# Kernel optimization log

Measured on AMD Instinct MI355X. Metric: run time of the kernel, lower is better.

Reference implementation:

```python
import jax, jax.numpy as jnp
import numpy as np

EMBED_DIM = 1024
NUM_HEADS = 16
HEAD_DIM = EMBED_DIM // NUM_HEADS
B, QL, CL = 2, 2048, 2048


def setup_inputs() -> dict:
    key = jax.random.key(0)
    ks = jax.random.split(key, 10)
    s = 1.0 / np.sqrt(EMBED_DIM)  # torch Linear default init scale (approx)
    inp = {
        "query": jax.random.normal(ks[0], (B, QL, EMBED_DIM), jnp.float32),
        "context": jax.random.normal(ks[1], (B, CL, EMBED_DIM), jnp.float32),
        "Wq": jax.random.normal(ks[2], (EMBED_DIM, EMBED_DIM), jnp.float32) * s,
        "bq": jnp.zeros((EMBED_DIM,), jnp.float32),
        "Wk": jax.random.normal(ks[3], (EMBED_DIM, EMBED_DIM), jnp.float32) * s,
        "bk": jnp.zeros((EMBED_DIM,), jnp.float32),
        "Wv": jax.random.normal(ks[4], (EMBED_DIM, EMBED_DIM), jnp.float32) * s,
        "bv": jnp.zeros((EMBED_DIM,), jnp.float32),
        "Wo": jax.random.normal(ks[5], (EMBED_DIM, EMBED_DIM), jnp.float32) * s,
        "bo": jnp.zeros((EMBED_DIM,), jnp.float32),
    }
    return inp


def reference(query, context, Wq, bq, Wk, bk, Wv, bv, Wo, bo):
    b, ql, _ = query.shape
    cl = context.shape[1]
    # projections (torch Linear: x @ W.T + b; here W stored as (in, out) so x @ W + b)
    Q = (query @ Wq + bq).reshape(b, ql, NUM_HEADS, HEAD_DIM).transpose(0, 2, 1, 3)
    K = (context @ Wk + bk).reshape(b, cl, NUM_HEADS, HEAD_DIM).transpose(0, 2, 1, 3)
    V = (context @ Wv + bv).reshape(b, cl, NUM_HEADS, HEAD_DIM).transpose(0, 2, 1, 3)
    # scores [b, h, ql, cl]
    scores = jnp.einsum("bhqd,bhkd->bhqk", Q, K) / np.sqrt(HEAD_DIM).astype(np.float32)
    probs = jax.nn.softmax(scores, axis=-1)
    # dropout=0.0 (eval): identity
    attended = jnp.einsum("bhqk,bhkd->bhqd", probs, V)
    attended = attended.transpose(0, 2, 1, 3).reshape(b, ql, EMBED_DIM)
    return attended @ Wo + bo
```

## Files before the change

### kernel.cpp

```cpp
#include <hip/hip_runtime.h>
#include <hip/hip_bf16.h>
#include <stdint.h>

#define EMBED 1024
#define NH 16
#define HD 64
#define BATCH 2
#define QLEN 2048
#define CLEN 2048

typedef short short8 __attribute__((ext_vector_type(8)));
typedef unsigned short ushort8v __attribute__((ext_vector_type(8)));
typedef float f32x4 __attribute__((ext_vector_type(4)));
typedef float f32x16 __attribute__((ext_vector_type(16)));
typedef uint32_t u32x4 __attribute__((ext_vector_type(4)));

#define QSCALE 0.18033688f

__device__ __forceinline__ void async_load16(const void* g, void* l) {
    __builtin_amdgcn_global_load_lds((const __attribute__((address_space(1))) void*)g,
                                     (__attribute__((address_space(3))) void*)l, 16, 0, 0);
}

__device__ __forceinline__ uint32_t pack2(float a, float b) {
    float2 f{a, b};
    __hip_bfloat162 t = __float22bfloat162_rn(f);
    uint32_t u;
    __builtin_memcpy(&u, &t, 4);
    return u;
}

__global__ void prep(const float* __restrict__ query, const float* __restrict__ context,
                     __hip_bfloat16* __restrict__ qbf, __hip_bfloat16* __restrict__ cbf,
                     const float* __restrict__ W0, const float* __restrict__ W1,
                     const float* __restrict__ W2, const float* __restrict__ W3,
                     __hip_bfloat16* __restrict__ T0, __hip_bfloat16* __restrict__ T1,
                     __hip_bfloat16* __restrict__ T2, __hip_bfloat16* __restrict__ T3) {
    const int y = blockIdx.y;
    const int tid = threadIdx.x;
    if (y < 2) {
        const float* src = y ? context : query;
        __hip_bfloat16* dst = y ? cbf : qbf;
#pragma unroll
        for (int k = 0; k < 4; k++) {
            const int i = (blockIdx.x * 1024 + k * 256 + tid) * 4;
            float4 v = *(const float4*)(src + i);
            __hip_bfloat16 h[4];
            h[0] = __float2bfloat16(v.x);
            h[1] = __float2bfloat16(v.y);
            h[2] = __float2bfloat16(v.z);
            h[3] = __float2bfloat16(v.w);
            *(ushort4*)(dst + i) = *(const ushort4*)h;
        }
    } else {
        const int z = y - 2;
        const float* W = z == 0 ? W0 : z == 1 ? W1 : z == 2 ? W2 : W3;
        __hip_bfloat16* Wt = z == 0 ? T0 : z == 1 ? T1 : z == 2 ? T2 : T3;
        __shared__ float t[32][33];
        const int tx = tid & 31, ty = tid >> 5;
        const int n0 = (blockIdx.x & 31) * 32, k0 = (blockIdx.x >> 5) * 32;
#pragma unroll
        for (int r = 0; r < 4; r++)
            t[ty * 4 + r][tx] = W[(size_t)(k0 + ty * 4 + r) * EMBED + n0 + tx];
        __syncthreads();
#pragma unroll
        for (int r = 0; r < 4; r++)
            Wt[(size_t)(n0 + ty * 4 + r) * EMBED + k0 + tx] = __float2bfloat16(t[tx][ty * 4 + r]);
    }
}

__device__ __forceinline__ void gemm128_acc(
    const __hip_bfloat16* __restrict__ A, const __hip_bfloat16* __restrict__ Bt,
    int m0, int n0, __hip_bfloat16* As, __hip_bfloat16* Bs, f32x4 acc[4][4]) {
    const int K = EMBED;
    const int tid = threadIdx.x;
    const int wave = __builtin_amdgcn_readfirstlane(tid >> 6);
    const int lane = tid & 63, l15 = lane & 15, quad = lane >> 4;
    const int wm = (wave >> 1) * 64, wn = (wave & 1) * 64;
    const int srow = tid >> 2, sseg = (tid & 3) * 8;
    for (int k0 = 0; k0 < K; k0 += 32) {
        __syncthreads();
#pragma unroll
        for (int s = 0; s < 2; s++) {
            async_load16(A + (size_t)(m0 + s * 64 + srow) * K + k0 + sseg,
                         As + (size_t)(s * 256 + wave * 64) * 8);
            async_load16(Bt + (size_t)(n0 + s * 64 + srow) * K + k0 + sseg,
                         Bs + (size_t)(s * 256 + wave * 64) * 8);
        }
        __syncthreads();
        short8 af[4], bf[4];
#pragma unroll
        for (int t = 0; t < 4; t++) {
            af[t] = *(const short8*)(As + (wm + t * 16 + l15) * 32 + quad * 8);
            bf[t] = *(const short8*)(Bs + (wn + t * 16 + l15) * 32 + quad * 8);
        }
#pragma unroll
        for (int mt = 0; mt < 4; mt++)
#pragma unroll
            for (int nt = 0; nt < 4; nt++)
                acc[mt][nt] = __builtin_amdgcn_mfma_f32_16x16x32_bf16(af[mt], bf[nt], acc[mt][nt], 0, 0, 0);
    }
}

__global__ __launch_bounds__(256, 3) void proj128(
    const __hip_bfloat16* __restrict__ qbf, const __hip_bfloat16* __restrict__ cbf,
    const __hip_bfloat16* __restrict__ Wqt, const __hip_bfloat16* __restrict__ Wkvt,
    const float* __restrict__ bq, const float* __restrict__ bk, const float* __restrict__ bv,
    __hip_bfloat16* __restrict__ Qp, __hip_bfloat16* __restrict__ Kp, __hip_bfloat16* __restrict__ Vtr) {
    __shared__ __hip_bfloat16 smem[8704];
    __hip_bfloat16* As = smem;
    __hip_bfloat16* Bs = smem + 4096;
    const int j = blockIdx.x;
    const int blk = (j & 7) * 96 + (j >> 3);
    const __hip_bfloat16 *A, *Bt;
    int m0, n0;
    if (blk < 256) {
        A = qbf; Bt = Wqt; m0 = (blk >> 3) * 128; n0 = (blk & 7) * 128;
    } else {
        const int f = blk - 256;
        A = cbf; Bt = Wkvt; m0 = (f >> 4) * 128; n0 = (f & 15) * 128;
    }
    f32x4 acc[4][4] = {};
    gemm128_acc(A, Bt, m0, n0, As, Bs, acc);

    const int tid = threadIdx.x;
    const int wave = __builtin_amdgcn_readfirstlane(tid >> 6);
    const int lane = tid & 63, l15 = lane & 15, quad = lane >> 4;
    const int wm = (wave >> 1) * 64, wn = (wave & 1) * 64;

    if (blk >= 256 && n0 >= 1024) {
        const int cb = n0 - 1024;
        const int b2 = m0 >> 11;
        const int tokb = m0 & 2047;
        __hip_bfloat16* T = smem;
#pragma unroll
        for (int hh = 0; hh < 2; hh++) {
            __syncthreads();
            if ((wn >> 6) == hh) {
#pragma unroll
                for (int nt = 0; nt < 4; nt++) {
                    const int cn = nt * 16 + l15;
                    const float bvv = bv[cb + hh * 64 + cn];
#pragma unroll
                    for (int mt = 0; mt < 4; mt++) {
                        const int m = wm + mt * 16 + quad * 4;
                        __hip_bfloat16 vb[4];
#pragma unroll
                        for (int r = 0; r < 4; r++) vb[r] = __float2bfloat16(acc[mt][nt][r] + bvv);
                        *(ushort4*)(T + cn * 136 + m) = *(const ushort4*)vb;
                    }
                }
            }
            __syncthreads();
            const int r = tid >> 2;
            const int seg = (tid & 3) * 32;
            unsigned short* dst = (unsigned short*)Vtr +
                (size_t)(b2 * 1024 + cb + hh * 64 + r) * CLEN + tokb + seg;
            const unsigned short* srcp = (const unsigned short*)(T + r * 136 + seg);
#pragma unroll
            for (int u = 0; u < 4; u++)
                *(ushort8v*)(dst + u * 8) = *(const ushort8v*)(srcp + u * 8);
        }
    } else {
        const bool isQ = (blk < 256);
        const float* bias = isQ ? bq : bk;
        __hip_bfloat16* C = isQ ? Qp : Kp;
        const float sc = isQ ? QSCALE : 1.0f;
#pragma unroll
        for (int mt = 0; mt < 4; mt++) {
#pragma unroll
            for (int nt = 0; nt < 4; nt++) {
                const int c = n0 + wn + nt * 16 + l15;
                const float bvv = bias[c];
                const int r0 = m0 + wm + mt * 16 + quad * 4;
#pragma unroll
                for (int r = 0; r < 4; r++)
                    C[(size_t)(r0 + r) * 1024 + c] = __float2bfloat16((acc[mt][nt][r] + bvv) * sc);
            }
        }
    }
}

__global__ __launch_bounds__(256, 4) void oproj(
    const __hip_bfloat16* __restrict__ A, const __hip_bfloat16* __restrict__ Bt,
    const float* __restrict__ bias, float* __restrict__ C) {
    __shared__ __hip_bfloat16 As[64 * 32];
    __shared__ __hip_bfloat16 Bs[128 * 32];
    const int K = EMBED, N = EMBED;
    const int j = blockIdx.x;
    const int L = (j & 7) * 64 + (j >> 3);
    const int m0 = (L >> 3) * 64, n0 = (L & 7) * 128;
    const int tid = threadIdx.x;
    const int wave = __builtin_amdgcn_readfirstlane(tid >> 6);
    const int lane = tid & 63, l15 = lane & 15, quad = lane >> 4;
    const int wm = (wave & 1) * 32, wn = (wave >> 1) * 64;
    const int srow = tid >> 2, sseg = (tid & 3) * 8;
    f32x4 acc[2][4] = {};
    for (int k0 = 0; k0 < K; k0 += 32) {
        __syncthreads();
        async_load16(A + (size_t)(m0 + srow) * K + k0 + sseg, As + (size_t)(wave * 64) * 8);
#pragma unroll
        for (int s = 0; s < 2; s++)
            async_load16(Bt + (size_t)(n0 + s * 64 + srow) * K + k0 + sseg,
                         Bs + (size_t)(s * 256 + wave * 64) * 8);
        __syncthreads();
        short8 af[2], bf[4];
#pragma unroll
        for (int t = 0; t < 2; t++)
            af[t] = *(const short8*)(As + (wm + t * 16 + l15) * 32 + quad * 8);
#pragma unroll
        for (int t = 0; t < 4; t++)
            bf[t] = *(const short8*)(Bs + (wn + t * 16 + l15) * 32 + quad * 8);
#pragma unroll
        for (int mt = 0; mt < 2; mt++)
#pragma unroll
            for (int nt = 0; nt < 4; nt++)
                acc[mt][nt] = __builtin_amdgcn_mfma_f32_16x16x32_bf16(af[mt], bf[nt], acc[mt][nt], 0, 0, 0);
    }
#pragma unroll
    for (int mt = 0; mt < 2; mt++) {
#pragma unroll
        for (int nt = 0; nt < 4; nt++) {
            const int c = n0 + wn + nt * 16 + l15;
            const float bvv = bias[c];
            const int r0 = m0 + wm + mt * 16 + quad * 4;
#pragma unroll
            for (int r = 0; r < 4; r++)
                C[(size_t)(r0 + r) * N + c] = acc[mt][nt][r] + bvv;
        }
    }
}

__global__ __launch_bounds__(256, 4) void flash_attn(
    const __hip_bfloat16* __restrict__ Q, const __hip_bfloat16* __restrict__ K,
    const __hip_bfloat16* __restrict__ Vt, __hip_bfloat16* __restrict__ O) {
    __shared__ __hip_bfloat16 Ks[2][64 * 64];
    __shared__ __hip_bfloat16 Vs[2][64 * 64];
    const int tid = threadIdx.x;
    const int wave = __builtin_amdgcn_readfirstlane(tid >> 6);
    const int wq = wave & 1, wc = wave >> 1;
    const int lane = tid & 63, l31 = lane & 31, hbit = lane >> 5;
    const int j = blockIdx.x;
    const int L = (j & 7) * 128 + (j >> 3);
    const int hy = L >> 5;
    const int b = hy >> 4, h = hy & 15;
    const int q0 = (L & 31) * 64;
    const size_t kbase = (size_t)b * CLEN * EMBED + (size_t)h * HD;
    const size_t vtbase = (size_t)((b * NH + h) * HD) * CLEN;
    const int srow8 = lane >> 3;
    const int sgb = (lane & 7) ^ srow8;
    __hip_bfloat16* stK = Ks[wc];
    __hip_bfloat16* stV = Vs[wc];

    const __hip_bfloat16* qptr =
        Q + (size_t)(b * QLEN + q0 + wq * 32 + l31) * EMBED + h * HD + hbit * 8;
    short8 qf[4];
#pragma unroll
    for (int t = 0; t < 4; t++) qf[t] = *(const short8*)(qptr + t * 16);

    f32x16 o[2] = {};
    float lsum = 0.f;
    const int cbase = wc * (CLEN / 2);

    for (int t = 0; t < 16; ++t) {
        const int c0 = cbase + t * 64;
        __syncthreads();
        if (wq == 0) {
#pragma unroll
            for (int i = 0; i < 8; i++)
                async_load16(K + kbase + (size_t)(c0 + i * 8 + srow8) * EMBED + (sgb ^ i) * 8,
                             stK + i * 512);
        } else {
#pragma unroll
            for (int i = 0; i < 8; i++)
                async_load16(Vt + vtbase + (size_t)(i * 8 + srow8) * CLEN + c0 + (sgb ^ i) * 8,
                             stV + i * 512);
        }
        __syncthreads();

#pragma unroll
        for (int mc = 0; mc < 2; mc++) {
            const int row = mc * 32 + l31;
            const int rsw = (row & 7) ^ (row >> 3);
            const __hip_bfloat16* kr = stK + row * 64;
            f32x16 s = {};
#pragma unroll
            for (int kc = 0; kc < 4; kc++) {
                short8 kf = *(const short8*)(kr + ((2 * kc + hbit) ^ rsw) * 8);
                s = __builtin_amdgcn_mfma_f32_32x32x16_bf16(kf, qf[kc], s, 0, 0, 0);
            }
            uint32_t dw[8];
#pragma unroll
            for (int i = 0; i < 8; i++) {
                const float p0 = __builtin_amdgcn_exp2f(s[2 * i]);
                const float p1 = __builtin_amdgcn_exp2f(s[2 * i + 1]);
                lsum += p0 + p1;
                dw[i] = pack2(p0, p1);
            }
#pragma unroll
            for (int tp = 0; tp < 2; tp++) {
                u32x4 fb;
#if __has_builtin(__builtin_amdgcn_permlane32_swap)
                {
                    auto s02 = __builtin_amdgcn_permlane32_swap(dw[4 * tp + 0], dw[4 * tp + 2], false, false);
                    auto s13 = __builtin_amdgcn_permlane32_swap(dw[4 * tp + 1], dw[4 * tp + 3], false, false);
                    fb[0] = s02[0];
                    fb[1] = s13[0];
                    fb[2] = s02[1];
                    fb[3] = s13[1];
                }
#else
                {
                    const uint32_t a0 = hbit ? dw[4 * tp + 2] : dw[4 * tp + 0];
                    const uint32_t a1 = hbit ? dw[4 * tp + 3] : dw[4 * tp + 1];
                    const uint32_t b0 = hbit ? dw[4 * tp + 0] : dw[4 * tp + 2];
                    const uint32_t b1 = hbit ? dw[4 * tp + 1] : dw[4 * tp + 3];
                    const uint32_t x0 = (uint32_t)__shfl_xor((int)b0, 32);
                    const uint32_t x1 = (uint32_t)__shfl_xor((int)b1, 32);
                    fb[0] = hbit ? x0 : a0;
                    fb[1] = hbit ? x1 : a1;
                    fb[2] = hbit ? a0 : x0;
                    fb[3] = hbit ? a1 : x1;
                }
#endif
                const short8 pfr = __builtin_bit_cast(short8, fb);
                const int kc2 = mc * 2 + tp;
#pragma unroll
                for (int dm = 0; dm < 2; dm++) {
                    const int vrow = dm * 32 + l31;
                    const int vsw = (vrow & 7) ^ (vrow >> 3);
                    short8 vf = *(const short8*)(stV + vrow * 64 + ((2 * kc2 + hbit) ^ vsw) * 8);
                    o[dm] = __builtin_amdgcn_mfma_f32_32x32x16_bf16(vf, pfr, o[dm], 0, 0, 0);
                }
            }
        }
    }

    __syncthreads();
    float4* scr4 = (float4*)&Ks[0][0];
    float* scrl = (float*)&Vs[0][0];
    if (wc == 1) {
#pragma unroll
        for (int i = 0; i < 8; i++) {
            float4 c4;
            c4.x = o[i >> 2][(i & 3) * 4 + 0];
            c4.y = o[i >> 2][(i & 3) * 4 + 1];
            c4.z = o[i >> 2][(i & 3) * 4 + 2];
            c4.w = o[i >> 2][(i & 3) * 4 + 3];
            scr4[i * 128 + wq * 64 + lane] = c4;
        }
        scrl[wq * 64 + lane] = lsum;
    }
    __syncthreads();
    if (wc == 0) {
        lsum += scrl[wq * 64 + lane];
#pragma unroll
        for (int i = 0; i < 8; i++) {
            float4 p = scr4[i * 128 + wq * 64 + lane];
            o[i >> 2][(i & 3) * 4 + 0] += p.x;
            o[i >> 2][(i & 3) * 4 + 1] += p.y;
            o[i >> 2][(i & 3) * 4 + 2] += p.z;
            o[i >> 2][(i & 3) * 4 + 3] += p.w;
        }
        lsum += __shfl_xor(lsum, 32);
        const float inv = 1.0f / lsum;
        const int q = q0 + wq * 32 + l31;
        __hip_bfloat16* orow = O + (size_t)(b * QLEN + q) * EMBED + h * HD;
#pragma unroll
        for (int dm = 0; dm < 2; dm++) {
#pragma unroll
            for (int g = 0; g < 4; g++) {
                __hip_bfloat16 ob[4];
#pragma unroll
                for (int r = 0; r < 4; r++) ob[r] = __float2bfloat16(o[dm][g * 4 + r] * inv);
                *(ushort4*)(orow + dm * 32 + hbit * 4 + g * 8) = *(const ushort4*)ob;
            }
        }
    }
}

extern "C" void kernel_launch(void* const* d_in, const int* in_sizes, int n_in,
                              void* d_out, int out_size, void* d_ws, size_t ws_size,
                              hipStream_t stream) {
    const float* query = (const float*)d_in[0];
    const float* context = (const float*)d_in[1];
    const float* Wq = (const float*)d_in[2];
    const float* bq = (const float*)d_in[3];
    const float* Wk = (const float*)d_in[4];
    const float* bk = (const float*)d_in[5];
    const float* Wv = (const float*)d_in[6];
    const float* bv = (const float*)d_in[7];
    const float* Wo = (const float*)d_in[8];
    const float* bo = (const float*)d_in[9];
    float* out = (float*)d_out;

    const int NTOK = BATCH * QLEN;
    const int NACT = NTOK * EMBED;
    const int NW = EMBED * EMBED;

    __hip_bfloat16* qbf = (__hip_bfloat16*)d_ws;
    __hip_bfloat16* cbf = qbf + NACT;
    __hip_bfloat16* Wqt = cbf + NACT;
    __hip_bfloat16* Wkt = Wqt + NW;
    __hip_bfloat16* Wvt = Wkt + NW;
    __hip_bfloat16* Wot = Wvt + NW;
    __hip_bfloat16* Qp = Wot + NW;
    __hip_bfloat16* Kp = Qp + NACT;
    __hip_bfloat16* Vtr = Kp + NACT;
    __hip_bfloat16* att = Vtr + NACT;

    prep<<<dim3(1024, 6), 256, 0, stream>>>(query, context, qbf, cbf,
                                            Wq, Wk, Wv, Wo, Wqt, Wkt, Wvt, Wot);

    proj128<<<768, 256, 0, stream>>>(qbf, cbf, Wqt, Wkt, bq, bk, bv, Qp, Kp, Vtr);

    flash_attn<<<1024, 256, 0, stream>>>(Qp, Kp, Vtr, att);

    oproj<<<512, 256, 0, stream>>>(att, Wot, bo, out);
}
```

Before: 207.2 us.

## Software-pipeline K/V tile loads across QK, softmax and PV phases

The attention loop is restructured so the next K tile is prefetched after the mid-iteration barrier, overlapping with the PV MFMAs. The V tile load is issued at the top of the iteration and overlaps the QK MFMAs and exp2 softmax work. The QK and PV phases are split, with both score tiles kept in registers. MFMA sections are wrapped in s_setprio raises to favour matrix-issue waves. This hides global-to-LDS load latency behind compute, at the cost of higher register pressure and reliance on barrier semantics for async-load visibility.

```diff
diff --git a/kernel.cpp b/kernel.cpp
--- a/kernel.cpp
+++ b/kernel.cpp
@@ -262,48 +262,72 @@
     float lsum = 0.f;
     const int cbase = wc * (CLEN / 2);
 
+    if (wq == 0) {
+#pragma unroll
+        for (int i = 0; i < 8; i++)
+            async_load16(K + kbase + (size_t)(cbase + i * 8 + srow8) * EMBED + (sgb ^ i) * 8,
+                         stK + i * 512);
+    }
+
     for (int t = 0; t < 16; ++t) {
         const int c0 = cbase + t * 64;
         __syncthreads();
-        if (wq == 0) {
-#pragma unroll
-            for (int i = 0; i < 8; i++)
-                async_load16(K + kbase + (size_t)(c0 + i * 8 + srow8) * EMBED + (sgb ^ i) * 8,
-                             stK + i * 512);
-        } else {
+        if (wq == 1) {
 #pragma unroll
             for (int i = 0; i < 8; i++)
                 async_load16(Vt + vtbase + (size_t)(i * 8 + srow8) * CLEN + c0 + (sgb ^ i) * 8,
                              stV + i * 512);
         }
-        __syncthreads();
-
+
+        f32x16 s[2];
+        __builtin_amdgcn_s_setprio(1);
 #pragma unroll
         for (int mc = 0; mc < 2; mc++) {
             const int row = mc * 32 + l31;
             const int rsw = (row & 7) ^ (row >> 3);
             const __hip_bfloat16* kr = stK + row * 64;
-            f32x16 s = {};
+            f32x16 sv = {};
 #pragma unroll
             for (int kc = 0; kc < 4; kc++) {
                 short8 kf = *(const short8*)(kr + ((2 * kc + hbit) ^ rsw) * 8);
-                s = __builtin_amdgcn_mfma_f32_32x32x16_bf16(kf, qf[kc], s, 0, 0, 0);
-            }
-            uint32_t dw[8];
+                sv = __builtin_amdgcn_mfma_f32_32x32x16_bf16(kf, qf[kc], sv, 0, 0, 0);
+            }
+            s[mc] = sv;
+        }
+        __builtin_amdgcn_s_setprio(0);
+
+        uint32_t dw[2][8];
+        float ls0 = 0.f, ls1 = 0.f;
+#pragma unroll
+        for (int mc = 0; mc < 2; mc++) {
 #pragma unroll
             for (int i = 0; i < 8; i++) {
-                const float p0 = __builtin_amdgcn_exp2f(s[2 * i]);
-                const float p1 = __builtin_amdgcn_exp2f(s[2 * i + 1]);
-                lsum += p0 + p1;
-                dw[i] = pack2(p0, p1);
-            }
+                const float p0 = __builtin_amdgcn_exp2f(s[mc][2 * i]);
+                const float p1 = __builtin_amdgcn_exp2f(s[mc][2 * i + 1]);
+                if (i & 1) ls1 += p0 + p1; else ls0 += p0 + p1;
+                dw[mc][i] = pack2(p0, p1);
+            }
+        }
+        lsum += ls0 + ls1;
+
+        __syncthreads();
+        if (wq == 0 && t < 15) {
+            const int cn = cbase + (t + 1) * 64;
+#pragma unroll
+            for (int i = 0; i < 8; i++)
+                async_load16(K + kbase + (size_t)(cn + i * 8 + srow8) * EMBED + (sgb ^ i) * 8,
+                             stK + i * 512);
+        }
+
+#pragma unroll
+        for (int mc = 0; mc < 2; mc++) {
 #pragma unroll
             for (int tp = 0; tp < 2; tp++) {
                 u32x4 fb;
 #if __has_builtin(__builtin_amdgcn_permlane32_swap)
                 {
-                    auto s02 = __builtin_amdgcn_permlane32_swap(dw[4 * tp + 0], dw[4 * tp + 2], false, false);
-                    auto s13 = __builtin_amdgcn_permlane32_swap(dw[4 * tp + 1], dw[4 * tp + 3], false, false);
+                    auto s02 = __builtin_amdgcn_permlane32_swap(dw[mc][4 * tp + 0], dw[mc][4 * tp + 2], false, false);
+                    auto s13 = __builtin_amdgcn_permlane32_swap(dw[mc][4 * tp + 1], dw[mc][4 * tp + 3], false, false);
                     fb[0] = s02[0];
                     fb[1] = s13[0];
                     fb[2] = s02[1];
@@ -311,10 +335,10 @@
                 }
 #else
                 {
-                    const uint32_t a0 = hbit ? dw[4 * tp + 2] : dw[4 * tp + 0];
-                    const uint32_t a1 = hbit ? dw[4 * tp + 3] : dw[4 * tp + 1];
-                    const uint32_t b0 = hbit ? dw[4 * tp + 0] : dw[4 * tp + 2];
-                    const uint32_t b1 = hbit ? dw[4 * tp + 1] : dw[4 * tp + 3];
+                    const uint32_t a0 = hbit ? dw[mc][4 * tp + 2] : dw[mc][4 * tp + 0];
+                    const uint32_t a1 = hbit ? dw[mc][4 * tp + 3] : dw[mc][4 * tp + 1];
+                    const uint32_t b0 = hbit ? dw[mc][4 * tp + 0] : dw[mc][4 * tp + 2];
+                    const uint32_t b1 = hbit ? dw[mc][4 * tp + 1] : dw[mc][4 * tp + 3];
                     const uint32_t x0 = (uint32_t)__shfl_xor((int)b0, 32);
                     const uint32_t x1 = (uint32_t)__shfl_xor((int)b1, 32);
                     fb[0] = hbit ? x0 : a0;
@@ -325,6 +349,7 @@
 #endif
                 const short8 pfr = __builtin_bit_cast(short8, fb);
                 const int kc2 = mc * 2 + tp;
+                __builtin_amdgcn_s_setprio(1);
 #pragma unroll
                 for (int dm = 0; dm < 2; dm++) {
                     const int vrow = dm * 32 + l31;
@@ -332,6 +357,7 @@
                     short8 vf = *(const short8*)(stV + vrow * 64 + ((2 * kc2 + hbit) ^ vsw) * 8);
                     o[dm] = __builtin_amdgcn_mfma_f32_32x32x16_bf16(vf, pfr, o[dm], 0, 0, 0);
                 }
+                __builtin_amdgcn_s_setprio(0);
             }
         }
     }
```

Result: slower. 227.6 us (+9.8%).

## Restructure flash attention to 128-query blocks with double-buffered K/V tiles

Applied to the files above, without the earlier changes.

Each block now handles 128 queries, one 32-row slice per wave, and every wave walks the full context. The old split of waves into two context halves is gone, along with its LDS cross-wave reduction, and the grid is halved. K/V tiles are double-buffered with a prefetch of the next tile issued before computing the current one, so only one barrier per iteration remains, and setprio is raised around the MFMA sections. This trades less parallelism per block and fewer blocks for better K/V reuse across more queries and overlap of loads with compute.

```diff
diff --git a/kernel.cpp b/kernel.cpp
--- a/kernel.cpp
+++ b/kernel.cpp
@@ -238,63 +238,71 @@
     __shared__ __hip_bfloat16 Vs[2][64 * 64];
     const int tid = threadIdx.x;
     const int wave = __builtin_amdgcn_readfirstlane(tid >> 6);
-    const int wq = wave & 1, wc = wave >> 1;
     const int lane = tid & 63, l31 = lane & 31, hbit = lane >> 5;
     const int j = blockIdx.x;
-    const int L = (j & 7) * 128 + (j >> 3);
-    const int hy = L >> 5;
+    const int L = (j & 7) * 64 + (j >> 3);
+    const int hy = L >> 4;
     const int b = hy >> 4, h = hy & 15;
-    const int q0 = (L & 31) * 64;
+    const int q0 = (L & 15) * 128;
     const size_t kbase = (size_t)b * CLEN * EMBED + (size_t)h * HD;
     const size_t vtbase = (size_t)((b * NH + h) * HD) * CLEN;
     const int srow8 = lane >> 3;
     const int sgb = (lane & 7) ^ srow8;
-    __hip_bfloat16* stK = Ks[wc];
-    __hip_bfloat16* stV = Vs[wc];
 
     const __hip_bfloat16* qptr =
-        Q + (size_t)(b * QLEN + q0 + wq * 32 + l31) * EMBED + h * HD + hbit * 8;
+        Q + (size_t)(b * QLEN + q0 + wave * 32 + l31) * EMBED + h * HD + hbit * 8;
     short8 qf[4];
 #pragma unroll
     for (int t = 0; t < 4; t++) qf[t] = *(const short8*)(qptr + t * 16);
 
     f32x16 o[2] = {};
-    float lsum = 0.f;
-    const int cbase = wc * (CLEN / 2);
-
-    for (int t = 0; t < 16; ++t) {
-        const int c0 = cbase + t * 64;
-        __syncthreads();
-        if (wq == 0) {
-#pragma unroll
-            for (int i = 0; i < 8; i++)
-                async_load16(K + kbase + (size_t)(c0 + i * 8 + srow8) * EMBED + (sgb ^ i) * 8,
-                             stK + i * 512);
-        } else {
-#pragma unroll
-            for (int i = 0; i < 8; i++)
-                async_load16(Vt + vtbase + (size_t)(i * 8 + srow8) * CLEN + c0 + (sgb ^ i) * 8,
-                             stV + i * 512);
-        }
-        __syncthreads();
+    float lsA = 0.f, lsB = 0.f;
+
+#pragma unroll
+    for (int u = 0; u < 2; u++) {
+        const int i = wave * 2 + u;
+        async_load16(K + kbase + (size_t)(i * 8 + srow8) * EMBED + (sgb ^ i) * 8,
+                     Ks[0] + i * 512);
+        async_load16(Vt + vtbase + (size_t)(i * 8 + srow8) * CLEN + (sgb ^ i) * 8,
+                     Vs[0] + i * 512);
+    }
+
+    for (int t = 0; t < 32; ++t) {
+        const int cur = t & 1;
+        __syncthreads();
+        if (t < 31) {
+            const int cn = (t + 1) * 64;
+#pragma unroll
+            for (int u = 0; u < 2; u++) {
+                const int i = wave * 2 + u;
+                async_load16(K + kbase + (size_t)(cn + i * 8 + srow8) * EMBED + (sgb ^ i) * 8,
+                             Ks[cur ^ 1] + i * 512);
+                async_load16(Vt + vtbase + (size_t)(i * 8 + srow8) * CLEN + cn + (sgb ^ i) * 8,
+                             Vs[cur ^ 1] + i * 512);
+            }
+        }
+        const __hip_bfloat16* stK = Ks[cur];
+        const __hip_bfloat16* stV = Vs[cur];
 
 #pragma unroll
         for (int mc = 0; mc < 2; mc++) {
             const int row = mc * 32 + l31;
             const int rsw = (row & 7) ^ (row >> 3);
             const __hip_bfloat16* kr = stK + row * 64;
-            f32x16 s = {};
+            f32x16 sv = {};
+            __builtin_amdgcn_s_setprio(1);
 #pragma unroll
             for (int kc = 0; kc < 4; kc++) {
                 short8 kf = *(const short8*)(kr + ((2 * kc + hbit) ^ rsw) * 8);
-                s = __builtin_amdgcn_mfma_f32_32x32x16_bf16(kf, qf[kc], s, 0, 0, 0);
-            }
+                sv = __builtin_amdgcn_mfma_f32_32x32x16_bf16(kf, qf[kc], sv, 0, 0, 0);
+            }
+            __builtin_amdgcn_s_setprio(0);
             uint32_t dw[8];
 #pragma unroll
             for (int i = 0; i < 8; i++) {
-                const float p0 = __builtin_amdgcn_exp2f(s[2 * i]);
-                const float p1 = __builtin_amdgcn_exp2f(s[2 * i + 1]);
-                lsum += p0 + p1;
+                const float p0 = __builtin_amdgcn_exp2f(sv[2 * i]);
+                const float p1 = __builtin_amdgcn_exp2f(sv[2 * i + 1]);
+                if (i & 1) lsB += p0 + p1; else lsA += p0 + p1;
                 dw[i] = pack2(p0, p1);
             }
 #pragma unroll
@@ -325,6 +333,7 @@
 #endif
                 const short8 pfr = __builtin_bit_cast(short8, fb);
                 const int kc2 = mc * 2 + tp;
+                __builtin_amdgcn_s_setprio(1);
 #pragma unroll
                 for (int dm = 0; dm < 2; dm++) {
                     const int vrow = dm * 32 + l31;
@@ -332,49 +341,24 @@
                     short8 vf = *(const short8*)(stV + vrow * 64 + ((2 * kc2 + hbit) ^ vsw) * 8);
                     o[dm] = __builtin_amdgcn_mfma_f32_32x32x16_bf16(vf, pfr, o[dm], 0, 0, 0);
                 }
-            }
-        }
-    }
-
-    __syncthreads();
-    float4* scr4 = (float4*)&Ks[0][0];
-    float* scrl = (float*)&Vs[0][0];
-    if (wc == 1) {
-#pragma unroll
-        for (int i = 0; i < 8; i++) {
-            float4 c4;
-            c4.x = o[i >> 2][(i & 3) * 4 + 0];
-            c4.y = o[i >> 2][(i & 3) * 4 + 1];
-            c4.z = o[i >> 2][(i & 3) * 4 + 2];
-            c4.w = o[i >> 2][(i & 3) * 4 + 3];
-            scr4[i * 128 + wq * 64 + lane] = c4;
-        }
-        scrl[wq * 64 + lane] = lsum;
-    }
-    __syncthreads();
-    if (wc == 0) {
-        lsum += scrl[wq * 64 + lane];
-#pragma unroll
-        for (int i = 0; i < 8; i++) {
-            float4 p = scr4[i * 128 + wq * 64 + lane];
-            o[i >> 2][(i & 3) * 4 + 0] += p.x;
-            o[i >> 2][(i & 3) * 4 + 1] += p.y;
-            o[i >> 2][(i & 3) * 4 + 2] += p.z;
-            o[i >> 2][(i & 3) * 4 + 3] += p.w;
-        }
-        lsum += __shfl_xor(lsum, 32);
-        const float inv = 1.0f / lsum;
-        const int q = q0 + wq * 32 + l31;
-        __hip_bfloat16* orow = O + (size_t)(b * QLEN + q) * EMBED + h * HD;
-#pragma unroll
-        for (int dm = 0; dm < 2; dm++) {
-#pragma unroll
-            for (int g = 0; g < 4; g++) {
-                __hip_bfloat16 ob[4];
-#pragma unroll
-                for (int r = 0; r < 4; r++) ob[r] = __float2bfloat16(o[dm][g * 4 + r] * inv);
-                *(ushort4*)(orow + dm * 32 + hbit * 4 + g * 8) = *(const ushort4*)ob;
-            }
+                __builtin_amdgcn_s_setprio(0);
+            }
+        }
+    }
+
+    float lsum = lsA + lsB;
+    lsum += __shfl_xor(lsum, 32);
+    const float inv = 1.0f / lsum;
+    const int q = q0 + wave * 32 + l31;
+    __hip_bfloat16* orow = O + (size_t)(b * QLEN + q) * EMBED + h * HD;
+#pragma unroll
+    for (int dm = 0; dm < 2; dm++) {
+#pragma unroll
+        for (int g = 0; g < 4; g++) {
+            __hip_bfloat16 ob[4];
+#pragma unroll
+            for (int r = 0; r < 4; r++) ob[r] = __float2bfloat16(o[dm][g * 4 + r] * inv);
+            *(ushort4*)(orow + dm * 32 + hbit * 4 + g * 8) = *(const ushort4*)ob;
         }
     }
 }
@@ -414,7 +398,7 @@
 
     proj128<<<768, 256, 0, stream>>>(qbf, cbf, Wqt, Wkt, bq, bk, bv, Qp, Kp, Vtr);
 
-    flash_attn<<<1024, 256, 0, stream>>>(Qp, Kp, Vtr, att);
+    flash_attn<<<512, 256, 0, stream>>>(Qp, Kp, Vtr, att);
 
     oproj<<<512, 256, 0, stream>>>(att, Wot, bo, out);
 }
```

Result: slower. 218.8 us (+5.6%).
